# Performance work log

Measured on AMD Instinct MI355X. Metric: run time of the kernel, lower is better.

Reference implementation:

```python
import jax, jax.numpy as jnp
import numpy as np

N_NODES = 100000
N_GRAPHS = 512
NEG_SLOPE = 0.2


def gat_layer(x, src, dst, W, a_src, a_dst, b):
    # PyG GATConv (heads=1, concat=True, add_self_loops handled by caller via src/dst)
    h = x @ W                                   # [N, F]
    e = jax.nn.leaky_relu((h @ a_src)[src] + (h @ a_dst)[dst], NEG_SLOPE)  # [E]
    m = jax.ops.segment_max(e, dst, num_segments=N_NODES)
    ex = jnp.exp(e - m[dst])
    s = jax.ops.segment_sum(ex, dst, num_segments=N_NODES)
    alpha = ex / (s[dst] + 1e-16)               # per-destination softmax
    out = jax.ops.segment_sum(alpha[:, None] * h[src], dst, num_segments=N_NODES)
    return out + b


def setup_inputs() -> dict:
    key = jax.random.key(0)
    ks = jax.random.split(key, 12)
    x = jax.random.normal(ks[0], (N_NODES, 5), dtype=jnp.float32)
    edge_index = jax.random.randint(ks[1], (2, 3200000), 0, N_NODES, dtype=jnp.int64)
    batch = jnp.sort(jax.random.randint(ks[2], (N_NODES,), 0, N_GRAPHS, dtype=jnp.int64))
    def glorot(k, shape):
        lim = float(np.sqrt(6.0 / (shape[0] + shape[-1])))
        return jax.random.uniform(k, shape, jnp.float32, -lim, lim)
    return {
        "x": x, "edge_index": edge_index, "batch": batch,
        "W1": glorot(ks[3], (5, 16)), "as1": glorot(ks[4], (16,)), "ad1": glorot(ks[5], (16,)), "b1": jnp.zeros((16,), jnp.float32),
        "W2": glorot(ks[6], (16, 16)), "as2": glorot(ks[7], (16,)), "ad2": glorot(ks[8], (16,)), "b2": jnp.zeros((16,), jnp.float32),
        "Wf": glorot(ks[9], (16, 2)), "bf": jnp.zeros((2,), jnp.float32),
    }


def reference(x, edge_index, batch, W1, as1, ad1, b1, W2, as2, ad2, b2, Wf, bf):
    # add self-loops (PyG GATConv default)
    loop = jnp.arange(N_NODES, dtype=edge_index.dtype)
    src = jnp.concatenate([edge_index[0], loop])
    dst = jnp.concatenate([edge_index[1], loop])
    h = jax.nn.relu(gat_layer(x, src, dst, W1, as1, ad1, b1))
    h = jax.nn.relu(gat_layer(h, src, dst, W2, as2, ad2, b2))
    # global mean pool over graphs
    sums = jax.ops.segment_sum(h, batch, num_segments=N_GRAPHS)
    cnt = jax.ops.segment_sum(jnp.ones((N_NODES,), h.dtype), batch, num_segments=N_GRAPHS)
    pooled = sums / jnp.maximum(cnt, 1.0)[:, None]   # [G, 16]
    return pooled @ Wf + bf                          # [G, 2]
```

## Files before the change

kernel.cpp:

```cpp
#include <hip/hip_runtime.h>
#include <hip/hip_fp16.h>
#include <math.h>

#define N_NODES 100000
#define N_GRAPHS 512
#define F 16
#define NEG_SLOPE 0.2f
#define DMAX 80
#define NSLOT 64
#define NBUCK 391
#define BCAP 8704
#define EPB 16
#define GPB 32

__device__ __forceinline__ float lrelu(float v) {
    return v > 0.0f ? v : NEG_SLOPE * v;
}

__device__ __forceinline__ unsigned fkey(float f) {
    unsigned b = __float_as_uint(f);
    return (b & 0x80000000u) ? ~b : (b | 0x80000000u);
}
__device__ __forceinline__ float funkey(unsigned k) {
    unsigned b = (k & 0x80000000u) ? (k ^ 0x80000000u) : ~k;
    return __uint_as_float(b);
}

__device__ __forceinline__ float pe_unpack(unsigned v) {
    return __half2float(__ushort_as_half((unsigned short)(v >> 17)));
}
__device__ __forceinline__ unsigned pe_pack(int s, float pe) {
    return (unsigned)s | ((unsigned)__half_as_ushort(__float2half(pe)) << 17);
}

__device__ __forceinline__ float slot_max_c(const unsigned* __restrict__ cs,
                                            const unsigned* __restrict__ cd) {
    unsigned ms = 0, md = 0;
#pragma unroll 8
    for (int i = 0; i < NSLOT; ++i) {
        ms = max(ms, cs[i]);
        md = max(md, cd[i]);
    }
    return lrelu(funkey(ms) + funkey(md));
}

__global__ void k_part_prep(const int* __restrict__ esrc,
                            const int* __restrict__ edst, int E0, int nT,
                            int* __restrict__ bcur,
                            unsigned* __restrict__ bucket,
                            const float* __restrict__ x,
                            const float* __restrict__ W1,
                            const float* __restrict__ as1,
                            const float* __restrict__ ad1,
                            __half* __restrict__ h1,
                            float* __restrict__ ssrc,
                            float* __restrict__ sdst,
                            unsigned* __restrict__ cs1,
                            unsigned* __restrict__ cd1) {
    __shared__ int hist[NBUCK];
    __shared__ int gbase[NBUCK];
    __shared__ int off[NBUCK];
    __shared__ unsigned ls[4], ld[4];

    if ((int)blockIdx.x < nT) {
        int tbase = blockIdx.x * (blockDim.x * EPB);
        for (int i = threadIdx.x; i < NBUCK; i += blockDim.x) hist[i] = 0;
        __syncthreads();

        int rb[EPB];
        unsigned rv[EPB];
#pragma unroll
        for (int i = 0; i < EPB; ++i) {
            int e = tbase + i * blockDim.x + threadIdx.x;
            rb[i] = -1;
            if (e < E0) {
                int d = edst[e];
                int s = esrc[e];
                int b = d >> 8;
                rb[i] = b;
                rv[i] = (unsigned)s | ((unsigned)(d & 255) << 17);
                atomicAdd(&hist[b], 1);
            }
        }
        __syncthreads();

        for (int b = threadIdx.x; b < NBUCK; b += blockDim.x) {
            int h = hist[b];
            gbase[b] = h ? atomicAdd(&bcur[b], h) : 0;
            off[b] = 0;
        }
        __syncthreads();

#pragma unroll
        for (int i = 0; i < EPB; ++i) {
            int b = rb[i];
            if (b >= 0) {
                int p = gbase[b] + atomicAdd(&off[b], 1);
                if (p < BCAP) bucket[(size_t)b * BCAP + p] = rv[i];
            }
        }
    } else {
        int n = (blockIdx.x - nT) * blockDim.x + threadIdx.x;
        float ss = -INFINITY, sd = -INFINITY;
        if (n < N_NODES) {
            float xi[5];
#pragma unroll
            for (int i = 0; i < 5; ++i) xi[i] = x[n * 5 + i];
            ss = 0.f; sd = 0.f;
#pragma unroll
            for (int f = 0; f < F; ++f) {
                float acc = 0.f;
#pragma unroll
                for (int i = 0; i < 5; ++i) acc += xi[i] * W1[i * F + f];
                h1[n * F + f] = __float2half(acc);
                ss += acc * as1[f];
                sd += acc * ad1[f];
            }
            ssrc[n] = ss;
            sdst[n] = sd;
        }
        unsigned ks = fkey(ss), kd = fkey(sd);
#pragma unroll
        for (int o = 32; o; o >>= 1) {
            ks = max(ks, (unsigned)__shfl_xor((int)ks, o, 64));
            kd = max(kd, (unsigned)__shfl_xor((int)kd, o, 64));
        }
        int wid = threadIdx.x >> 6, lane = threadIdx.x & 63;
        if (lane == 0) { ls[wid] = ks; ld[wid] = kd; }
        __syncthreads();
        if (threadIdx.x == 0) {
            unsigned ms = ls[0], md = ld[0];
#pragma unroll
            for (int w = 1; w < 4; ++w) { ms = max(ms, ls[w]); md = max(md, ld[w]); }
            atomicMax(&cs1[blockIdx.x & (NSLOT - 1)], ms);
            atomicMax(&cd1[blockIdx.x & (NSLOT - 1)], md);
        }
    }
}

__global__ void k_fill2(const int* __restrict__ bcur,
                        const unsigned* __restrict__ bucket,
                        const float* __restrict__ ssrc1,
                        const float* __restrict__ sdst1,
                        const unsigned* __restrict__ cs1,
                        const unsigned* __restrict__ cd1,
                        unsigned* __restrict__ col,
                        int* __restrict__ deg) {
    int b = blockIdx.x;
    __shared__ int cur[256];
    __shared__ float sdl[256];
    if (threadIdx.x < 256) {
        cur[threadIdx.x] = 0;
        int dst = (b << 8) | threadIdx.x;
        sdl[threadIdx.x] = (dst < N_NODES) ? sdst1[dst] : 0.f;
    }
    __syncthreads();
    float c1 = slot_max_c(cs1, cd1);
    int cnt = min(bcur[b], BCAP);
    const unsigned* bk = bucket + (size_t)b * BCAP;
    for (int i = threadIdx.x; i < cnt; i += blockDim.x) {
        unsigned v = __builtin_nontemporal_load(&bk[i]);
        int s = (int)(v & 0x1FFFFu);
        int dl = (int)(v >> 17);
        int r = atomicAdd(&cur[dl], 1);
        if (r < DMAX) {
            float pe = __expf(lrelu(ssrc1[s] + sdl[dl]) - c1);
            col[((size_t)((b << 8) | dl)) * DMAX + r] = pe_pack(s, pe);
        }
    }
    __syncthreads();
    if (threadIdx.x < 256) {
        int dst = (b << 8) | threadIdx.x;
        if (dst < N_NODES) deg[dst] = min(cur[threadIdx.x], DMAX);
    }
}

__device__ __forceinline__ float2 gat_agg8(int n, int l,
                                           const int* __restrict__ deg,
                                           const unsigned* __restrict__ col,
                                           const float* __restrict__ ssrc,
                                           const float* __restrict__ sdst,
                                           const unsigned* __restrict__ hX,
                                           const float* __restrict__ b,
                                           float c) {
    int dg = deg[n];
    size_t st = (size_t)n * DMAX;
    float ax = 0.f, ay = 0.f, ssum = 0.f;
    int base = 0;
    for (; base + 8 <= dg; base += 8) {
        unsigned v = __builtin_nontemporal_load(&col[st + base + l]);
        ssum += pe_unpack(v);
#pragma unroll
        for (int k = 0; k < 8; ++k) {
            unsigned vk = __shfl(v, k, 8);
            int sk = (int)(vk & 0x1FFFFu);
            float pk = pe_unpack(vk);
            unsigned hw = hX[sk * 8 + l];
            ax += pk * __half2float(__ushort_as_half((unsigned short)(hw & 0xFFFFu)));
            ay += pk * __half2float(__ushort_as_half((unsigned short)(hw >> 16)));
        }
    }
    if (base < dg) {
        int j = base + l;
        unsigned v = 0;
        if (j < dg) {
            v = __builtin_nontemporal_load(&col[st + j]);
            ssum += pe_unpack(v);
        }
        int cnt = dg - base;
        for (int k = 0; k < cnt; ++k) {
            unsigned vk = __shfl(v, k, 8);
            int sk = (int)(vk & 0x1FFFFu);
            float pk = pe_unpack(vk);
            unsigned hw = hX[sk * 8 + l];
            ax += pk * __half2float(__ushort_as_half((unsigned short)(hw & 0xFFFFu)));
            ay += pk * __half2float(__ushort_as_half((unsigned short)(hw >> 16)));
        }
    }
#pragma unroll
    for (int o = 1; o < 8; o <<= 1) ssum += __shfl_xor(ssum, o, 8);
    float pes = __expf(lrelu(ssrc[n] + sdst[n]) - c);
    unsigned hw = hX[n * 8 + l];
    ax += pes * __half2float(__ushort_as_half((unsigned short)(hw & 0xFFFFu)));
    ay += pes * __half2float(__ushort_as_half((unsigned short)(hw >> 16)));
    ssum += pes;
    float inv = 1.f / (ssum + 1e-16f);
    float2 of;
    of.x = fmaxf(ax * inv + b[2 * l], 0.f);
    of.y = fmaxf(ay * inv + b[2 * l + 1], 0.f);
    return of;
}

__global__ void k_gather1(const int* __restrict__ deg,
                          const unsigned* __restrict__ col,
                          const float* __restrict__ ssrc1,
                          const float* __restrict__ sdst1,
                          const unsigned* __restrict__ h1x,
                          const float* __restrict__ b1,
                          const float* __restrict__ W2,
                          const float* __restrict__ as2,
                          const float* __restrict__ ad2,
                          unsigned* __restrict__ h2x,
                          float* __restrict__ ssrc2,
                          float* __restrict__ sdst2,
                          const unsigned* __restrict__ cs1,
                          const unsigned* __restrict__ cd1,
                          unsigned* __restrict__ cs2,
                          unsigned* __restrict__ cd2) {
    __shared__ float lho[GPB][17];
    __shared__ unsigned ls[4], ld[4];
    int gid = threadIdx.x >> 3;
    int l = threadIdx.x & 7;
    int n = blockIdx.x * GPB + gid;

    float c1 = slot_max_c(cs1, cd1);
    float2 of = gat_agg8(n, l, deg, col, ssrc1, sdst1, h1x, b1, c1);

    lho[gid][2 * l] = of.x;
    lho[gid][2 * l + 1] = of.y;

    float hx = 0.f, hy = 0.f;
#pragma unroll
    for (int i = 0; i < 16; ++i) {
        float hoi = lho[gid][i];
        hx += hoi * W2[i * F + 2 * l];
        hy += hoi * W2[i * F + 2 * l + 1];
    }
    h2x[n * 8 + l] = (unsigned)__half_as_ushort(__float2half(hx)) |
                     ((unsigned)__half_as_ushort(__float2half(hy)) << 16);

    float ps = hx * as2[2 * l] + hy * as2[2 * l + 1];
    float pd = hx * ad2[2 * l] + hy * ad2[2 * l + 1];
#pragma unroll
    for (int o = 1; o < 8; o <<= 1) {
        ps += __shfl_xor(ps, o, 8);
        pd += __shfl_xor(pd, o, 8);
    }
    if (l == 0) { ssrc2[n] = ps; sdst2[n] = pd; }

    unsigned ks = fkey(ps), kd = fkey(pd);
#pragma unroll
    for (int o = 8; o < 64; o <<= 1) {
        ks = max(ks, (unsigned)__shfl_xor((int)ks, o, 64));
        kd = max(kd, (unsigned)__shfl_xor((int)kd, o, 64));
    }
    int wid = threadIdx.x >> 6, wl = threadIdx.x & 63;
    if (wl == 0) { ls[wid] = ks; ld[wid] = kd; }
    __syncthreads();
    if (threadIdx.x == 0) {
        unsigned ms = max(max(ls[0], ls[1]), max(ls[2], ls[3]));
        unsigned md = max(max(ld[0], ld[1]), max(ld[2], ld[3]));
        atomicMax(&cs2[blockIdx.x & (NSLOT - 1)], ms);
        atomicMax(&cd2[blockIdx.x & (NSLOT - 1)], md);
    }
}

__global__ void k_pe2(const int* __restrict__ deg,
                      unsigned* __restrict__ col,
                      const float* __restrict__ ssrc2,
                      const float* __restrict__ sdst2,
                      const unsigned* __restrict__ cs2,
                      const unsigned* __restrict__ cd2) {
    int gid = threadIdx.x >> 3;
    int l = threadIdx.x & 7;
    int n = blockIdx.x * GPB + gid;
    float c2 = slot_max_c(cs2, cd2);
    int dg = deg[n];
    size_t st = (size_t)n * DMAX;
    float sd = sdst2[n];
    for (int j = l; j < dg; j += 8) {
        unsigned v = col[st + j];
        int s = (int)(v & 0x1FFFFu);
        float pe = __expf(lrelu(ssrc2[s] + sd) - c2);
        col[st + j] = pe_pack(s, pe);
    }
}

__global__ void k_gather2(const int* __restrict__ deg,
                          const unsigned* __restrict__ col,
                          const float* __restrict__ ssrc2,
                          const float* __restrict__ sdst2,
                          const unsigned* __restrict__ h2x,
                          const float* __restrict__ b2,
                          const int* __restrict__ batch,
                          float* __restrict__ gsum,
                          float* __restrict__ gcnt,
                          const unsigned* __restrict__ cs2,
                          const unsigned* __restrict__ cd2) {
    __shared__ float pool[4 * F];
    __shared__ float pcnt[4];
    if (threadIdx.x < 4 * F) pool[threadIdx.x] = 0.f;
    if (threadIdx.x < 4) pcnt[threadIdx.x] = 0.f;
    __syncthreads();

    int gid = threadIdx.x >> 3;
    int l = threadIdx.x & 7;
    int n = blockIdx.x * GPB + gid;

    float c2 = slot_max_c(cs2, cd2);
    float2 of = gat_agg8(n, l, deg, col, ssrc2, sdst2, h2x, b2, c2);

    int g = batch[n];
    int g0 = batch[blockIdx.x * GPB];
    int idx = g - g0;
    if (idx < 4) {
        atomicAdd(&pool[idx * F + 2 * l], of.x);
        atomicAdd(&pool[idx * F + 2 * l + 1], of.y);
        if (l == 0) atomicAdd(&pcnt[idx], 1.f);
    } else {
        atomicAdd(&gsum[g * F + 2 * l], of.x);
        atomicAdd(&gsum[g * F + 2 * l + 1], of.y);
        if (l == 0) atomicAdd(&gcnt[g], 1.f);
    }
    __syncthreads();
    if (threadIdx.x < 4 * F) {
        float v = pool[threadIdx.x];
        if (v != 0.f)
            atomicAdd(&gsum[(g0 + (threadIdx.x >> 4)) * F + (threadIdx.x & 15)], v);
    }
    if (threadIdx.x < 4) {
        float cv = pcnt[threadIdx.x];
        if (cv != 0.f) atomicAdd(&gcnt[g0 + threadIdx.x], cv);
    }
}

__global__ void k_final(const float* __restrict__ gsum,
                        const float* __restrict__ gcnt,
                        const float* __restrict__ Wf,
                        const float* __restrict__ bf,
                        float* __restrict__ out) {
    int g = blockIdx.x * blockDim.x + threadIdx.x;
    if (g >= N_GRAPHS) return;
    float inv = 1.f / fmaxf(gcnt[g], 1.f);
    float o0 = bf[0], o1 = bf[1];
#pragma unroll
    for (int i = 0; i < F; ++i) {
        float p = gsum[g * F + i] * inv;
        o0 += p * Wf[i * 2 + 0];
        o1 += p * Wf[i * 2 + 1];
    }
    out[g * 2 + 0] = o0;
    out[g * 2 + 1] = o1;
}

extern "C" void kernel_launch(void* const* d_in, const int* in_sizes, int n_in,
                              void* d_out, int out_size, void* d_ws, size_t ws_size,
                              hipStream_t stream) {
    const float* x   = (const float*)d_in[0];
    const int*   ei  = (const int*)d_in[1];
    const int*   bat = (const int*)d_in[2];
    const float* W1  = (const float*)d_in[3];
    const float* as1 = (const float*)d_in[4];
    const float* ad1 = (const float*)d_in[5];
    const float* b1  = (const float*)d_in[6];
    const float* W2  = (const float*)d_in[7];
    const float* as2 = (const float*)d_in[8];
    const float* ad2 = (const float*)d_in[9];
    const float* b2  = (const float*)d_in[10];
    const float* Wf  = (const float*)d_in[11];
    const float* bf  = (const float*)d_in[12];
    float* out = (float*)d_out;

    const int E0 = in_sizes[1] / 2;
    const int* esrc = ei;
    const int* edst = ei + E0;

    __half* h1   = (__half*)d_ws;
    __half* h2   = h1 + (size_t)N_NODES * F;
    float* ssrc1 = (float*)(h2 + (size_t)N_NODES * F);
    float* sdst1 = ssrc1 + N_NODES;
    float* ssrc2 = sdst1 + N_NODES;
    float* sdst2 = ssrc2 + N_NODES;
    unsigned* col = (unsigned*)(sdst2 + N_NODES);
    int*   deg   = (int*)(col + (size_t)N_NODES * DMAX);
    unsigned* bucket = (unsigned*)(deg + N_NODES);
    int*      zbase = (int*)(bucket + (size_t)NBUCK * BCAP);
    int*      bcur  = zbase;
    unsigned* cs1   = (unsigned*)(bcur + NBUCK);
    unsigned* cd1   = cs1 + NSLOT;
    unsigned* cs2   = cd1 + NSLOT;
    unsigned* cd2   = cs2 + NSLOT;
    float*    gsum  = (float*)(cd2 + NSLOT);
    float*    gcnt  = gsum + (size_t)N_GRAPHS * F;
    size_t zbytes = (size_t)(NBUCK + 4 * NSLOT + N_GRAPHS * F + N_GRAPHS) * 4;

    hipMemsetAsync(zbase, 0, zbytes, stream);

    const int BT = 256;
    const int nT = (E0 + BT * EPB - 1) / (BT * EPB);
    const int nN = (N_NODES + BT - 1) / BT;
    dim3 bPP(nT + nN);
    dim3 bB(NBUCK);
    dim3 bW(N_NODES / GPB);
    dim3 bG((N_GRAPHS + BT - 1) / BT);

    k_part_prep<<<bPP, BT, 0, stream>>>(esrc, edst, E0, nT, bcur, bucket,
                                        x, W1, as1, ad1, h1, ssrc1, sdst1, cs1, cd1);
    k_fill2<<<bB, 1024, 0, stream>>>(bcur, bucket, ssrc1, sdst1, cs1, cd1, col, deg);
    k_gather1<<<bW, BT, 0, stream>>>(deg, col, ssrc1, sdst1, (const unsigned*)h1, b1,
                                     W2, as2, ad2, (unsigned*)h2, ssrc2, sdst2,
                                     cs1, cd1, cs2, cd2);
    k_pe2<<<bW, BT, 0, stream>>>(deg, col, ssrc2, sdst2, cs2, cd2);
    k_gather2<<<bW, BT, 0, stream>>>(deg, col, ssrc2, sdst2, (const unsigned*)h2, b2,
                                     bat, gsum, gcnt, cs2, cd2);
    k_final<<<bG, BT, 0, stream>>>(gsum, gcnt, Wf, bf, out);
}
```

Baseline: 273.4 us.

## Fuse all GAT stages into one cooperative persistent kernel with grid syncs

Replaces the memset and six separate kernel launches with a single cooperative kernel of 256 blocks × 1024 threads. The stages are separated by grid-wide syncs, and each block loops over work items with a grid stride. The goal is to remove launch overhead and the gaps between kernels. In exchange, parallelism is capped at 256 blocks of 1024 threads, which may lower occupancy and latency hiding in the gather phases. Each grid.sync also adds its own cost.

```diff
diff --git a/kernel.cpp b/kernel.cpp
--- a/kernel.cpp
+++ b/kernel.cpp
@@ -1,6 +1,9 @@
 #include <hip/hip_runtime.h>
 #include <hip/hip_fp16.h>
+#include <hip/hip_cooperative_groups.h>
 #include <math.h>
+
+namespace cg = cooperative_groups;
 
 #define N_NODES 100000
 #define N_GRAPHS 512
@@ -10,13 +13,15 @@
 #define NSLOT 64
 #define NBUCK 391
 #define BCAP 8704
-#define EPB 16
-#define GPB 32
+#define NBLK 256
+#define BT 1024
+#define EPB 4
+#define GPB 128
+#define NCHUNK ((N_NODES + GPB - 1) / GPB)
 
 __device__ __forceinline__ float lrelu(float v) {
     return v > 0.0f ? v : NEG_SLOPE * v;
 }
-
 __device__ __forceinline__ unsigned fkey(float f) {
     unsigned b = __float_as_uint(f);
     return (b & 0x80000000u) ? ~b : (b | 0x80000000u);
@@ -25,14 +30,12 @@
     unsigned b = (k & 0x80000000u) ? (k ^ 0x80000000u) : ~k;
     return __uint_as_float(b);
 }
-
 __device__ __forceinline__ float pe_unpack(unsigned v) {
     return __half2float(__ushort_as_half((unsigned short)(v >> 17)));
 }
 __device__ __forceinline__ unsigned pe_pack(int s, float pe) {
     return (unsigned)s | ((unsigned)__half_as_ushort(__float2half(pe)) << 17);
 }
-
 __device__ __forceinline__ float slot_max_c(const unsigned* __restrict__ cs,
                                             const unsigned* __restrict__ cd) {
     unsigned ms = 0, md = 0;
@@ -42,137 +45,6 @@
         md = max(md, cd[i]);
     }
     return lrelu(funkey(ms) + funkey(md));
-}
-
-__global__ void k_part_prep(const int* __restrict__ esrc,
-                            const int* __restrict__ edst, int E0, int nT,
-                            int* __restrict__ bcur,
-                            unsigned* __restrict__ bucket,
-                            const float* __restrict__ x,
-                            const float* __restrict__ W1,
-                            const float* __restrict__ as1,
-                            const float* __restrict__ ad1,
-                            __half* __restrict__ h1,
-                            float* __restrict__ ssrc,
-                            float* __restrict__ sdst,
-                            unsigned* __restrict__ cs1,
-                            unsigned* __restrict__ cd1) {
-    __shared__ int hist[NBUCK];
-    __shared__ int gbase[NBUCK];
-    __shared__ int off[NBUCK];
-    __shared__ unsigned ls[4], ld[4];
-
-    if ((int)blockIdx.x < nT) {
-        int tbase = blockIdx.x * (blockDim.x * EPB);
-        for (int i = threadIdx.x; i < NBUCK; i += blockDim.x) hist[i] = 0;
-        __syncthreads();
-
-        int rb[EPB];
-        unsigned rv[EPB];
-#pragma unroll
-        for (int i = 0; i < EPB; ++i) {
-            int e = tbase + i * blockDim.x + threadIdx.x;
-            rb[i] = -1;
-            if (e < E0) {
-                int d = edst[e];
-                int s = esrc[e];
-                int b = d >> 8;
-                rb[i] = b;
-                rv[i] = (unsigned)s | ((unsigned)(d & 255) << 17);
-                atomicAdd(&hist[b], 1);
-            }
-        }
-        __syncthreads();
-
-        for (int b = threadIdx.x; b < NBUCK; b += blockDim.x) {
-            int h = hist[b];
-            gbase[b] = h ? atomicAdd(&bcur[b], h) : 0;
-            off[b] = 0;
-        }
-        __syncthreads();
-
-#pragma unroll
-        for (int i = 0; i < EPB; ++i) {
-            int b = rb[i];
-            if (b >= 0) {
-                int p = gbase[b] + atomicAdd(&off[b], 1);
-                if (p < BCAP) bucket[(size_t)b * BCAP + p] = rv[i];
-            }
-        }
-    } else {
-        int n = (blockIdx.x - nT) * blockDim.x + threadIdx.x;
-        float ss = -INFINITY, sd = -INFINITY;
-        if (n < N_NODES) {
-            float xi[5];
-#pragma unroll
-            for (int i = 0; i < 5; ++i) xi[i] = x[n * 5 + i];
-            ss = 0.f; sd = 0.f;
-#pragma unroll
-            for (int f = 0; f < F; ++f) {
-                float acc = 0.f;
-#pragma unroll
-                for (int i = 0; i < 5; ++i) acc += xi[i] * W1[i * F + f];
-                h1[n * F + f] = __float2half(acc);
-                ss += acc * as1[f];
-                sd += acc * ad1[f];
-            }
-            ssrc[n] = ss;
-            sdst[n] = sd;
-        }
-        unsigned ks = fkey(ss), kd = fkey(sd);
-#pragma unroll
-        for (int o = 32; o; o >>= 1) {
-            ks = max(ks, (unsigned)__shfl_xor((int)ks, o, 64));
-            kd = max(kd, (unsigned)__shfl_xor((int)kd, o, 64));
-        }
-        int wid = threadIdx.x >> 6, lane = threadIdx.x & 63;
-        if (lane == 0) { ls[wid] = ks; ld[wid] = kd; }
-        __syncthreads();
-        if (threadIdx.x == 0) {
-            unsigned ms = ls[0], md = ld[0];
-#pragma unroll
-            for (int w = 1; w < 4; ++w) { ms = max(ms, ls[w]); md = max(md, ld[w]); }
-            atomicMax(&cs1[blockIdx.x & (NSLOT - 1)], ms);
-            atomicMax(&cd1[blockIdx.x & (NSLOT - 1)], md);
-        }
-    }
-}
-
-__global__ void k_fill2(const int* __restrict__ bcur,
-                        const unsigned* __restrict__ bucket,
-                        const float* __restrict__ ssrc1,
-                        const float* __restrict__ sdst1,
-                        const unsigned* __restrict__ cs1,
-                        const unsigned* __restrict__ cd1,
-                        unsigned* __restrict__ col,
-                        int* __restrict__ deg) {
-    int b = blockIdx.x;
-    __shared__ int cur[256];
-    __shared__ float sdl[256];
-    if (threadIdx.x < 256) {
-        cur[threadIdx.x] = 0;
-        int dst = (b << 8) | threadIdx.x;
-        sdl[threadIdx.x] = (dst < N_NODES) ? sdst1[dst] : 0.f;
-    }
-    __syncthreads();
-    float c1 = slot_max_c(cs1, cd1);
-    int cnt = min(bcur[b], BCAP);
-    const unsigned* bk = bucket + (size_t)b * BCAP;
-    for (int i = threadIdx.x; i < cnt; i += blockDim.x) {
-        unsigned v = __builtin_nontemporal_load(&bk[i]);
-        int s = (int)(v & 0x1FFFFu);
-        int dl = (int)(v >> 17);
-        int r = atomicAdd(&cur[dl], 1);
-        if (r < DMAX) {
-            float pe = __expf(lrelu(ssrc1[s] + sdl[dl]) - c1);
-            col[((size_t)((b << 8) | dl)) * DMAX + r] = pe_pack(s, pe);
-        }
-    }
-    __syncthreads();
-    if (threadIdx.x < 256) {
-        int dst = (b << 8) | threadIdx.x;
-        if (dst < N_NODES) deg[dst] = min(cur[threadIdx.x], DMAX);
-    }
 }
 
 __device__ __forceinline__ float2 gat_agg8(int n, int l,
@@ -231,156 +103,261 @@
     return of;
 }
 
-__global__ void k_gather1(const int* __restrict__ deg,
-                          const unsigned* __restrict__ col,
-                          const float* __restrict__ ssrc1,
-                          const float* __restrict__ sdst1,
-                          const unsigned* __restrict__ h1x,
-                          const float* __restrict__ b1,
-                          const float* __restrict__ W2,
-                          const float* __restrict__ as2,
-                          const float* __restrict__ ad2,
-                          unsigned* __restrict__ h2x,
-                          float* __restrict__ ssrc2,
-                          float* __restrict__ sdst2,
-                          const unsigned* __restrict__ cs1,
-                          const unsigned* __restrict__ cd1,
-                          unsigned* __restrict__ cs2,
-                          unsigned* __restrict__ cd2) {
-    __shared__ float lho[GPB][17];
-    __shared__ unsigned ls[4], ld[4];
-    int gid = threadIdx.x >> 3;
-    int l = threadIdx.x & 7;
-    int n = blockIdx.x * GPB + gid;
-
-    float c1 = slot_max_c(cs1, cd1);
-    float2 of = gat_agg8(n, l, deg, col, ssrc1, sdst1, h1x, b1, c1);
-
-    lho[gid][2 * l] = of.x;
-    lho[gid][2 * l + 1] = of.y;
-
-    float hx = 0.f, hy = 0.f;
-#pragma unroll
-    for (int i = 0; i < 16; ++i) {
-        float hoi = lho[gid][i];
-        hx += hoi * W2[i * F + 2 * l];
-        hy += hoi * W2[i * F + 2 * l + 1];
-    }
-    h2x[n * 8 + l] = (unsigned)__half_as_ushort(__float2half(hx)) |
-                     ((unsigned)__half_as_ushort(__float2half(hy)) << 16);
-
-    float ps = hx * as2[2 * l] + hy * as2[2 * l + 1];
-    float pd = hx * ad2[2 * l] + hy * ad2[2 * l + 1];
-#pragma unroll
-    for (int o = 1; o < 8; o <<= 1) {
-        ps += __shfl_xor(ps, o, 8);
-        pd += __shfl_xor(pd, o, 8);
-    }
-    if (l == 0) { ssrc2[n] = ps; sdst2[n] = pd; }
-
-    unsigned ks = fkey(ps), kd = fkey(pd);
-#pragma unroll
-    for (int o = 8; o < 64; o <<= 1) {
-        ks = max(ks, (unsigned)__shfl_xor((int)ks, o, 64));
-        kd = max(kd, (unsigned)__shfl_xor((int)kd, o, 64));
-    }
-    int wid = threadIdx.x >> 6, wl = threadIdx.x & 63;
-    if (wl == 0) { ls[wid] = ks; ld[wid] = kd; }
-    __syncthreads();
-    if (threadIdx.x == 0) {
-        unsigned ms = max(max(ls[0], ls[1]), max(ls[2], ls[3]));
-        unsigned md = max(max(ld[0], ld[1]), max(ld[2], ld[3]));
-        atomicMax(&cs2[blockIdx.x & (NSLOT - 1)], ms);
-        atomicMax(&cd2[blockIdx.x & (NSLOT - 1)], md);
-    }
-}
-
-__global__ void k_pe2(const int* __restrict__ deg,
-                      unsigned* __restrict__ col,
-                      const float* __restrict__ ssrc2,
-                      const float* __restrict__ sdst2,
-                      const unsigned* __restrict__ cs2,
-                      const unsigned* __restrict__ cd2) {
-    int gid = threadIdx.x >> 3;
-    int l = threadIdx.x & 7;
-    int n = blockIdx.x * GPB + gid;
-    float c2 = slot_max_c(cs2, cd2);
-    int dg = deg[n];
-    size_t st = (size_t)n * DMAX;
-    float sd = sdst2[n];
-    for (int j = l; j < dg; j += 8) {
-        unsigned v = col[st + j];
-        int s = (int)(v & 0x1FFFFu);
-        float pe = __expf(lrelu(ssrc2[s] + sd) - c2);
-        col[st + j] = pe_pack(s, pe);
-    }
-}
-
-__global__ void k_gather2(const int* __restrict__ deg,
-                          const unsigned* __restrict__ col,
-                          const float* __restrict__ ssrc2,
-                          const float* __restrict__ sdst2,
-                          const unsigned* __restrict__ h2x,
-                          const float* __restrict__ b2,
-                          const int* __restrict__ batch,
-                          float* __restrict__ gsum,
-                          float* __restrict__ gcnt,
-                          const unsigned* __restrict__ cs2,
-                          const unsigned* __restrict__ cd2) {
-    __shared__ float pool[4 * F];
-    __shared__ float pcnt[4];
-    if (threadIdx.x < 4 * F) pool[threadIdx.x] = 0.f;
-    if (threadIdx.x < 4) pcnt[threadIdx.x] = 0.f;
-    __syncthreads();
-
-    int gid = threadIdx.x >> 3;
-    int l = threadIdx.x & 7;
-    int n = blockIdx.x * GPB + gid;
-
-    float c2 = slot_max_c(cs2, cd2);
-    float2 of = gat_agg8(n, l, deg, col, ssrc2, sdst2, h2x, b2, c2);
-
-    int g = batch[n];
-    int g0 = batch[blockIdx.x * GPB];
-    int idx = g - g0;
-    if (idx < 4) {
-        atomicAdd(&pool[idx * F + 2 * l], of.x);
-        atomicAdd(&pool[idx * F + 2 * l + 1], of.y);
-        if (l == 0) atomicAdd(&pcnt[idx], 1.f);
-    } else {
-        atomicAdd(&gsum[g * F + 2 * l], of.x);
-        atomicAdd(&gsum[g * F + 2 * l + 1], of.y);
-        if (l == 0) atomicAdd(&gcnt[g], 1.f);
-    }
-    __syncthreads();
-    if (threadIdx.x < 4 * F) {
-        float v = pool[threadIdx.x];
-        if (v != 0.f)
-            atomicAdd(&gsum[(g0 + (threadIdx.x >> 4)) * F + (threadIdx.x & 15)], v);
-    }
-    if (threadIdx.x < 4) {
-        float cv = pcnt[threadIdx.x];
-        if (cv != 0.f) atomicAdd(&gcnt[g0 + threadIdx.x], cv);
-    }
-}
-
-__global__ void k_final(const float* __restrict__ gsum,
-                        const float* __restrict__ gcnt,
-                        const float* __restrict__ Wf,
-                        const float* __restrict__ bf,
-                        float* __restrict__ out) {
-    int g = blockIdx.x * blockDim.x + threadIdx.x;
-    if (g >= N_GRAPHS) return;
-    float inv = 1.f / fmaxf(gcnt[g], 1.f);
-    float o0 = bf[0], o1 = bf[1];
-#pragma unroll
-    for (int i = 0; i < F; ++i) {
-        float p = gsum[g * F + i] * inv;
-        o0 += p * Wf[i * 2 + 0];
-        o1 += p * Wf[i * 2 + 1];
-    }
-    out[g * 2 + 0] = o0;
-    out[g * 2 + 1] = o1;
+__global__ __launch_bounds__(BT, 4) void k_mega(
+        const int* __restrict__ esrc, const int* __restrict__ edst,
+        int E0, int nT, int nPrep,
+        int* __restrict__ bcur, unsigned* __restrict__ bucket,
+        const float* __restrict__ x, const float* __restrict__ W1,
+        const float* __restrict__ as1, const float* __restrict__ ad1,
+        unsigned* __restrict__ h1x, float* __restrict__ ssrc1,
+        float* __restrict__ sdst1, unsigned* __restrict__ cs1,
+        unsigned* __restrict__ cd1,
+        unsigned* __restrict__ col, int* __restrict__ deg,
+        const float* __restrict__ b1, const float* __restrict__ W2,
+        const float* __restrict__ as2, const float* __restrict__ ad2,
+        unsigned* __restrict__ h2x, float* __restrict__ ssrc2,
+        float* __restrict__ sdst2, unsigned* __restrict__ cs2,
+        unsigned* __restrict__ cd2,
+        const int* __restrict__ bat, float* __restrict__ gsum,
+        float* __restrict__ gcnt,
+        const float* __restrict__ b2, const float* __restrict__ Wf,
+        const float* __restrict__ bf, float* __restrict__ out,
+        int* __restrict__ zbase, int nzero) {
+    cg::grid_group grid = cg::this_grid();
+    const int tid = threadIdx.x;
+    const int bid = blockIdx.x;
+    __shared__ alignas(16) char smem[GPB * 17 * 4];
+
+    for (int i = bid * BT + tid; i < nzero; i += NBLK * BT) zbase[i] = 0;
+    grid.sync();
+
+    {
+        int* hist  = (int*)smem;
+        int* gbase = hist + NBUCK;
+        int* off   = gbase + NBUCK;
+        for (int w = bid; w < nT + nPrep; w += NBLK) {
+            if (w < nT) {
+                __syncthreads();
+                int tbase = w * (BT * EPB);
+                if (tid < NBUCK) hist[tid] = 0;
+                __syncthreads();
+                int rb[EPB]; unsigned rv[EPB];
+#pragma unroll
+                for (int i = 0; i < EPB; ++i) {
+                    int e = tbase + i * BT + tid;
+                    rb[i] = -1;
+                    if (e < E0) {
+                        int d = edst[e], s = esrc[e];
+                        rb[i] = d >> 8;
+                        rv[i] = (unsigned)s | ((unsigned)(d & 255) << 17);
+                        atomicAdd(&hist[rb[i]], 1);
+                    }
+                }
+                __syncthreads();
+                if (tid < NBUCK) {
+                    int h = hist[tid];
+                    gbase[tid] = h ? atomicAdd(&bcur[tid], h) : 0;
+                    off[tid] = 0;
+                }
+                __syncthreads();
+#pragma unroll
+                for (int i = 0; i < EPB; ++i) {
+                    int b = rb[i];
+                    if (b >= 0) {
+                        int p = gbase[b] + atomicAdd(&off[b], 1);
+                        if (p < BCAP) bucket[(size_t)b * BCAP + p] = rv[i];
+                    }
+                }
+            } else {
+                int n = (w - nT) * BT + tid;
+                float ss = -INFINITY, sd = -INFINITY;
+                if (n < N_NODES) {
+                    float xi[5];
+#pragma unroll
+                    for (int i = 0; i < 5; ++i) xi[i] = x[n * 5 + i];
+                    ss = 0.f; sd = 0.f;
+#pragma unroll
+                    for (int f = 0; f < F; ++f) {
+                        float acc = 0.f;
+#pragma unroll
+                        for (int i = 0; i < 5; ++i) acc += xi[i] * W1[i * F + f];
+                        ((__half*)h1x)[n * F + f] = __float2half(acc);
+                        ss += acc * as1[f];
+                        sd += acc * ad1[f];
+                    }
+                    ssrc1[n] = ss;
+                    sdst1[n] = sd;
+                }
+                unsigned ks = fkey(ss), kd = fkey(sd);
+#pragma unroll
+                for (int o = 32; o; o >>= 1) {
+                    ks = max(ks, (unsigned)__shfl_xor((int)ks, o, 64));
+                    kd = max(kd, (unsigned)__shfl_xor((int)kd, o, 64));
+                }
+                if ((tid & 63) == 0) {
+                    int slot = (w * 16 + (tid >> 6)) & (NSLOT - 1);
+                    atomicMax(&cs1[slot], ks);
+                    atomicMax(&cd1[slot], kd);
+                }
+            }
+        }
+    }
+    grid.sync();
+
+    {
+        int* cur   = (int*)smem;
+        float* sdl = (float*)(cur + 256);
+        float c1 = slot_max_c(cs1, cd1);
+        for (int b = bid; b < NBUCK; b += NBLK) {
+            if (tid < 256) {
+                cur[tid] = 0;
+                int dst = (b << 8) | tid;
+                sdl[tid] = (dst < N_NODES) ? sdst1[dst] : 0.f;
+            }
+            __syncthreads();
+            int cnt = min(bcur[b], BCAP);
+            const unsigned* bk = bucket + (size_t)b * BCAP;
+            for (int i = tid; i < cnt; i += BT) {
+                unsigned v = __builtin_nontemporal_load(&bk[i]);
+                int s = (int)(v & 0x1FFFFu);
+                int dl = (int)(v >> 17);
+                int r = atomicAdd(&cur[dl], 1);
+                if (r < DMAX) {
+                    float pe = __expf(lrelu(ssrc1[s] + sdl[dl]) - c1);
+                    col[((size_t)((b << 8) | dl)) * DMAX + r] = pe_pack(s, pe);
+                }
+            }
+            __syncthreads();
+            if (tid < 256) {
+                int dst = (b << 8) | tid;
+                if (dst < N_NODES) deg[dst] = min(cur[tid], DMAX);
+            }
+        }
+    }
+    grid.sync();
+
+    {
+        float (*lho)[17] = (float (*)[17])smem;
+        float c1 = slot_max_c(cs1, cd1);
+        int gid = tid >> 3, l = tid & 7;
+        for (int c = bid; c < NCHUNK; c += NBLK) {
+            int n = c * GPB + gid;
+            bool valid = n < N_NODES;
+            int nc = valid ? n : 0;
+            float2 of = gat_agg8(nc, l, deg, col, ssrc1, sdst1, h1x, b1, c1);
+            lho[gid][2 * l] = of.x;
+            lho[gid][2 * l + 1] = of.y;
+            float hx = 0.f, hy = 0.f;
+#pragma unroll
+            for (int i = 0; i < 16; ++i) {
+                float hoi = lho[gid][i];
+                hx += hoi * W2[i * F + 2 * l];
+                hy += hoi * W2[i * F + 2 * l + 1];
+            }
+            float ps = hx * as2[2 * l] + hy * as2[2 * l + 1];
+            float pd = hx * ad2[2 * l] + hy * ad2[2 * l + 1];
+#pragma unroll
+            for (int o = 1; o < 8; o <<= 1) {
+                ps += __shfl_xor(ps, o, 8);
+                pd += __shfl_xor(pd, o, 8);
+            }
+            if (valid) {
+                h2x[n * 8 + l] = (unsigned)__half_as_ushort(__float2half(hx)) |
+                                 ((unsigned)__half_as_ushort(__float2half(hy)) << 16);
+                if (l == 0) { ssrc2[n] = ps; sdst2[n] = pd; }
+            } else {
+                ps = -INFINITY; pd = -INFINITY;
+            }
+            unsigned ks = fkey(ps), kd = fkey(pd);
+#pragma unroll
+            for (int o = 8; o < 64; o <<= 1) {
+                ks = max(ks, (unsigned)__shfl_xor((int)ks, o, 64));
+                kd = max(kd, (unsigned)__shfl_xor((int)kd, o, 64));
+            }
+            if ((tid & 63) == 0) {
+                int slot = (c * 16 + (tid >> 6)) & (NSLOT - 1);
+                atomicMax(&cs2[slot], ks);
+                atomicMax(&cd2[slot], kd);
+            }
+        }
+    }
+    grid.sync();
+
+    {
+        float c2 = slot_max_c(cs2, cd2);
+        int gid = tid >> 3, l = tid & 7;
+        for (int c = bid; c < NCHUNK; c += NBLK) {
+            int n = c * GPB + gid;
+            if (n < N_NODES) {
+                int dg = deg[n];
+                size_t st = (size_t)n * DMAX;
+                float sd = sdst2[n];
+                for (int j = l; j < dg; j += 8) {
+                    unsigned v = col[st + j];
+                    int s = (int)(v & 0x1FFFFu);
+                    float pe = __expf(lrelu(ssrc2[s] + sd) - c2);
+                    col[st + j] = pe_pack(s, pe);
+                }
+            }
+        }
+    }
+    grid.sync();
+
+    {
+        float* pool = (float*)smem;
+        float* pcnt = pool + 4 * F;
+        float c2 = slot_max_c(cs2, cd2);
+        int gid = tid >> 3, l = tid & 7;
+        for (int c = bid; c < NCHUNK; c += NBLK) {
+            if (tid < 4 * F) pool[tid] = 0.f;
+            if (tid < 4) pcnt[tid] = 0.f;
+            __syncthreads();
+            int n = c * GPB + gid;
+            bool valid = n < N_NODES;
+            int nc = valid ? n : 0;
+            float2 of = gat_agg8(nc, l, deg, col, ssrc2, sdst2, h2x, b2, c2);
+            int g0 = bat[c * GPB];
+            if (valid) {
+                int g = bat[n];
+                int idx = g - g0;
+                if (idx < 4) {
+                    atomicAdd(&pool[idx * F + 2 * l], of.x);
+                    atomicAdd(&pool[idx * F + 2 * l + 1], of.y);
+                    if (l == 0) atomicAdd(&pcnt[idx], 1.f);
+                } else {
+                    atomicAdd(&gsum[g * F + 2 * l], of.x);
+                    atomicAdd(&gsum[g * F + 2 * l + 1], of.y);
+                    if (l == 0) atomicAdd(&gcnt[g], 1.f);
+                }
+            }
+            __syncthreads();
+            if (tid < 4 * F) {
+                float v = pool[tid];
+                if (v != 0.f)
+                    atomicAdd(&gsum[(g0 + (tid >> 4)) * F + (tid & 15)], v);
+            }
+            if (tid < 4) {
+                float cv = pcnt[tid];
+                if (cv != 0.f) atomicAdd(&gcnt[g0 + tid], cv);
+            }
+            __syncthreads();
+        }
+    }
+    grid.sync();
+
+    if (bid == 0 && tid < N_GRAPHS) {
+        int g = tid;
+        float inv = 1.f / fmaxf(gcnt[g], 1.f);
+        float o0 = bf[0], o1 = bf[1];
+#pragma unroll
+        for (int i = 0; i < F; ++i) {
+            float p = gsum[g * F + i] * inv;
+            o0 += p * Wf[i * 2 + 0];
+            o1 += p * Wf[i * 2 + 1];
+        }
+        out[g * 2 + 0] = o0;
+        out[g * 2 + 1] = o1;
+    }
 }
 
 extern "C" void kernel_launch(void* const* d_in, const int* in_sizes, int n_in,
@@ -401,13 +378,13 @@
     const float* bf  = (const float*)d_in[12];
     float* out = (float*)d_out;
 
-    const int E0 = in_sizes[1] / 2;
+    int E0 = in_sizes[1] / 2;
     const int* esrc = ei;
     const int* edst = ei + E0;
 
-    __half* h1   = (__half*)d_ws;
-    __half* h2   = h1 + (size_t)N_NODES * F;
-    float* ssrc1 = (float*)(h2 + (size_t)N_NODES * F);
+    unsigned* h1x  = (unsigned*)d_ws;
+    unsigned* h2x  = h1x + (size_t)N_NODES * 8;
+    float* ssrc1 = (float*)(h2x + (size_t)N_NODES * 8);
     float* sdst1 = ssrc1 + N_NODES;
     float* ssrc2 = sdst1 + N_NODES;
     float* sdst2 = ssrc2 + N_NODES;
@@ -422,26 +399,23 @@
     unsigned* cd2   = cs2 + NSLOT;
     float*    gsum  = (float*)(cd2 + NSLOT);
     float*    gcnt  = gsum + (size_t)N_GRAPHS * F;
-    size_t zbytes = (size_t)(NBUCK + 4 * NSLOT + N_GRAPHS * F + N_GRAPHS) * 4;
-
-    hipMemsetAsync(zbase, 0, zbytes, stream);
-
-    const int BT = 256;
-    const int nT = (E0 + BT * EPB - 1) / (BT * EPB);
-    const int nN = (N_NODES + BT - 1) / BT;
-    dim3 bPP(nT + nN);
-    dim3 bB(NBUCK);
-    dim3 bW(N_NODES / GPB);
-    dim3 bG((N_GRAPHS + BT - 1) / BT);
-
-    k_part_prep<<<bPP, BT, 0, stream>>>(esrc, edst, E0, nT, bcur, bucket,
-                                        x, W1, as1, ad1, h1, ssrc1, sdst1, cs1, cd1);
-    k_fill2<<<bB, 1024, 0, stream>>>(bcur, bucket, ssrc1, sdst1, cs1, cd1, col, deg);
-    k_gather1<<<bW, BT, 0, stream>>>(deg, col, ssrc1, sdst1, (const unsigned*)h1, b1,
-                                     W2, as2, ad2, (unsigned*)h2, ssrc2, sdst2,
-                                     cs1, cd1, cs2, cd2);
-    k_pe2<<<bW, BT, 0, stream>>>(deg, col, ssrc2, sdst2, cs2, cd2);
-    k_gather2<<<bW, BT, 0, stream>>>(deg, col, ssrc2, sdst2, (const unsigned*)h2, b2,
-                                     bat, gsum, gcnt, cs2, cd2);
-    k_final<<<bG, BT, 0, stream>>>(gsum, gcnt, Wf, bf, out);
-}
+    int nzero = NBUCK + 4 * NSLOT + N_GRAPHS * F + N_GRAPHS;
+
+    int nT = (E0 + BT * EPB - 1) / (BT * EPB);
+    int nPrep = (N_NODES + BT - 1) / BT;
+
+    void* args[] = {
+        (void*)&esrc, (void*)&edst, (void*)&E0, (void*)&nT, (void*)&nPrep,
+        (void*)&bcur, (void*)&bucket,
+        (void*)&x, (void*)&W1, (void*)&as1, (void*)&ad1,
+        (void*)&h1x, (void*)&ssrc1, (void*)&sdst1, (void*)&cs1, (void*)&cd1,
+        (void*)&col, (void*)&deg,
+        (void*)&b1, (void*)&W2, (void*)&as2, (void*)&ad2,
+        (void*)&h2x, (void*)&ssrc2, (void*)&sdst2, (void*)&cs2, (void*)&cd2,
+        (void*)&bat, (void*)&gsum, (void*)&gcnt,
+        (void*)&b2, (void*)&Wf, (void*)&bf, (void*)&out,
+        (void*)&zbase, (void*)&nzero
+    };
+    hipLaunchCooperativeKernel((void*)k_mega, dim3(NBLK), dim3(BT),
+                               args, 0, stream);
+}
```

Measured after the change: 527.1 us. 1.93x slower.
